# Performance work log

Hardware: AMD Instinct MI355X
Metric: run time of the kernel (lower is better)

## Reference

```python
import jax, jax.numpy as jnp
import numpy as np

B, S, D, H = 4, 2048, 768, 12
HD = D // H
SCALE = HD ** -0.5


def setup_inputs() -> dict:
    key = jax.random.key(0)
    ks = jax.random.split(key, 10)
    inp = {
        "x": jax.random.normal(ks[0], (B, S, D), jnp.float32),
        "attn_mask": jax.random.normal(ks[1], (B, S), jnp.float32),
        "Wq": jax.random.normal(ks[2], (D, D), jnp.float32) * (D ** -0.5),
        "bq": jax.random.normal(ks[3], (D,), jnp.float32) * 0.02,
        "Wk": jax.random.normal(ks[4], (D, D), jnp.float32) * (D ** -0.5),
        "bk": jax.random.normal(ks[5], (D,), jnp.float32) * 0.02,
        "Wv": jax.random.normal(ks[6], (D, D), jnp.float32) * (D ** -0.5),
        "bv": jax.random.normal(ks[7], (D,), jnp.float32) * 0.02,
        "Wo": jax.random.normal(ks[8], (D, D), jnp.float32) * (D ** -0.5),
        "bo": jax.random.normal(ks[9], (D,), jnp.float32) * 0.02,
    }
    return inp


def _split_heads(e):
    # [B, S, D] -> [B, H, S, HD]
    return e.reshape(B, S, H, HD).transpose(0, 2, 1, 3)


def reference(x, attn_mask, Wq, bq, Wk, bk, Wv, bv, Wo, bo):
    q = _split_heads((x @ Wq + bq) * SCALE)          # [B,H,S,HD]
    k = _split_heads(x @ Wk + bk)                     # [B,H,S,HD]
    v = _split_heads(x @ Wv + bv)                     # [B,H,S,HD]
    scores = jnp.einsum('bhsd,bhtd->bhst', q, k)      # [B,H,S,S]
    scores = scores + attn_mask[:, None, None, :]     # additive mask over keys
    probs = jax.nn.softmax(scores, axis=-1)
    out = jnp.einsum('bhst,bhtd->bhsd', probs, v)     # [B,H,S,HD]
    out = out.transpose(0, 2, 1, 3).reshape(B, S, D)  # merge heads
    return out @ Wo + bo
```

## Files before the change

kernel.cpp:

```cpp
#include <hip/hip_runtime.h>
#include <cmath>

#define B_ 4
#define S_ 2048
#define D_ 768
#define H_ 12
#define HD_ 64
#define SCALE_ 0.125f
#define LOG2E_ 1.4426950408889634f
#define M_ 8192

typedef unsigned short ushortT;
typedef unsigned int u32;
typedef __attribute__((ext_vector_type(8))) __bf16 bf16x8;
typedef __attribute__((ext_vector_type(4))) float f32x4;
typedef __attribute__((ext_vector_type(16))) float f32x16;

typedef __attribute__((address_space(1))) const void glb_cv;
typedef __attribute__((address_space(3))) void lds_v;

__device__ inline ushortT f2bf(float f) {
    return __builtin_bit_cast(ushortT, (__bf16)f);
}

__device__ inline u32 pk2bf(float a, float b) {
    return (u32)__builtin_bit_cast(ushortT, (__bf16)a)
         | ((u32)__builtin_bit_cast(ushortT, (__bf16)b) << 16);
}

__device__ inline float sum2bf(u32 u) {
    return __builtin_bit_cast(float, u << 16)
         + __builtin_bit_cast(float, u & 0xffff0000u);
}

__device__ inline void gload_lds16(const void* g, void* l) {
    __builtin_amdgcn_global_load_lds((glb_cv*)g, (lds_v*)l, 16, 0, 0);
}

__global__ __launch_bounds__(256)
void convert_f32_bf16(const float* __restrict__ in, ushortT* __restrict__ out)
{
    const size_t i = ((size_t)blockIdx.x * 256 + threadIdx.x) * 8;
    float4 a = *(const float4*)(in + i);
    float4 b = *(const float4*)(in + i + 4);
    union { ushortT u[8]; float4 f; } o;
    o.u[0] = f2bf(a.x); o.u[1] = f2bf(a.y); o.u[2] = f2bf(a.z); o.u[3] = f2bf(a.w);
    o.u[4] = f2bf(b.x); o.u[5] = f2bf(b.y); o.u[6] = f2bf(b.z); o.u[7] = f2bf(b.w);
    *(float4*)(out + i) = o.f;
}

__global__ __launch_bounds__(256)
void scale_mask(const float* __restrict__ in, float* __restrict__ outp)
{
    const int i = blockIdx.x * 256 + threadIdx.x;
    outp[i] = in[i] * LOG2E_;
}

__global__ __launch_bounds__(256)
void transpose_w(const float* __restrict__ W0, const float* __restrict__ W1,
                 const float* __restrict__ W2, const float* __restrict__ W3,
                 ushortT* __restrict__ wt4)
{
    const float* W = (blockIdx.z == 0) ? W0 : (blockIdx.z == 1) ? W1
                   : (blockIdx.z == 2) ? W2 : W3;
    ushortT* o = wt4 + (size_t)blockIdx.z * 768 * 768;
    __shared__ float T[64][65];
    const int tid = threadIdx.x;
    const int k0 = blockIdx.x * 64, n0 = blockIdx.y * 64;

    for (int t = tid; t < 1024; t += 256) {
        const int r = t >> 4, c4 = (t & 15) << 2;
        float4 v = *(const float4*)&W[(size_t)(k0 + r) * 768 + n0 + c4];
        T[r][c4 + 0] = v.x; T[r][c4 + 1] = v.y;
        T[r][c4 + 2] = v.z; T[r][c4 + 3] = v.w;
    }
    __syncthreads();
    for (int t = tid; t < 1024; t += 256) {
        const int r = t >> 4, c4 = (t & 15) << 2;
        union { ushortT u[4]; unsigned long long v; } ov;
        ov.u[0] = f2bf(T[c4 + 0][r]); ov.u[1] = f2bf(T[c4 + 1][r]);
        ov.u[2] = f2bf(T[c4 + 2][r]); ov.u[3] = f2bf(T[c4 + 3][r]);
        *(unsigned long long*)&o[(size_t)(n0 + r) * 768 + k0 + c4] = ov.v;
    }
}

__device__ inline void gemm_core_128x64(
    const ushortT* __restrict__ A, const ushortT* __restrict__ Bt,
    ushortT* As, ushortT* Bs, int m0, int n0, f32x4 acc[4][2])
{
    const int tid  = threadIdx.x;
    const int lane = tid & 63;
    const int wave = tid >> 6;
    const int lr = lane & 15, lg = lane >> 4;
    const int wr = wave >> 1, wc = wave & 1;

    #pragma unroll
    for (int mi = 0; mi < 4; ++mi)
        #pragma unroll
        for (int ni = 0; ni < 2; ++ni)
            acc[mi][ni] = (f32x4){0.f, 0.f, 0.f, 0.f};

    #pragma unroll 1
    for (int k0 = 0; k0 < 768; k0 += 64) {
        __syncthreads();
        #pragma unroll
        for (int it = 0; it < 4; ++it) {
            const int ci = it * 256 + tid;
            const int row = ci >> 3, c = ci & 7;
            const int sc = c ^ (row & 7);
            gload_lds16(A + (size_t)(m0 + row) * 768 + k0 + sc * 8,
                        As + (size_t)(it * 256 + wave * 64) * 8);
        }
        #pragma unroll
        for (int it = 0; it < 2; ++it) {
            const int ci = it * 256 + tid;
            const int row = ci >> 3, c = ci & 7;
            const int sc = c ^ (row & 7);
            gload_lds16(Bt + (size_t)(n0 + row) * 768 + k0 + sc * 8,
                        Bs + (size_t)(it * 256 + wave * 64) * 8);
        }
        __syncthreads();

        #pragma unroll
        for (int ks = 0; ks < 2; ++ks) {
            bf16x8 af[4], bfr[2];
            #pragma unroll
            for (int mi = 0; mi < 4; ++mi) {
                const int row = wr * 64 + mi * 16 + lr;
                const int ch = (ks * 4 + lg) ^ (row & 7);
                af[mi] = __builtin_bit_cast(bf16x8, *(const float4*)(As + row * 64 + ch * 8));
            }
            #pragma unroll
            for (int ni = 0; ni < 2; ++ni) {
                const int row = wc * 32 + ni * 16 + lr;
                const int ch = (ks * 4 + lg) ^ (row & 7);
                bfr[ni] = __builtin_bit_cast(bf16x8, *(const float4*)(Bs + row * 64 + ch * 8));
            }
            #pragma unroll
            for (int mi = 0; mi < 4; ++mi)
                #pragma unroll
                for (int ni = 0; ni < 2; ++ni)
                    acc[mi][ni] = __builtin_amdgcn_mfma_f32_16x16x32_bf16(
                        af[mi], bfr[ni], acc[mi][ni], 0, 0, 0);
        }
    }
}

__global__ __launch_bounds__(256)
void qkv_gemm(const ushortT* __restrict__ xb, const ushortT* __restrict__ wt4,
              const float* __restrict__ bq, const float* __restrict__ bk,
              const float* __restrict__ bv,
              ushortT* __restrict__ qb, ushortT* __restrict__ kb,
              ushortT* __restrict__ vtb)
{
    __shared__ __align__(16) ushortT As[128 * 64];
    __shared__ __align__(16) ushortT Bs[64 * 64];
    const int z = blockIdx.z;
    const ushortT* Wt = wt4 + (size_t)z * 768 * 768;
    const float* bias = (z == 0) ? bq : (z == 1) ? bk : bv;
    const float scale = (z == 0) ? (SCALE_ * LOG2E_) : 1.0f;

    const int m0 = blockIdx.x * 128, n0 = blockIdx.y * 64;
    f32x4 acc[4][2];
    gemm_core_128x64(xb, Wt, As, Bs, m0, n0, acc);

    const int tid = threadIdx.x;
    const int lane = tid & 63, wave = tid >> 6;
    const int lr = lane & 15, lg = lane >> 4;
    const int wr = wave >> 1, wc = wave & 1;
    const int h = n0 >> 6;

    if (z == 2) {
        #pragma unroll
        for (int ni = 0; ni < 2; ++ni) {
            const int nn = wc * 32 + ni * 16 + lr;
            const float bb = bias[n0 + nn];
            #pragma unroll
            for (int mi = 0; mi < 4; ++mi) {
                const int mb = m0 + wr * 64 + mi * 16 + lg * 4;
                const int b = mb >> 11, s = mb & 2047;
                ushort4 ov;
                ov.x = f2bf(acc[mi][ni][0] + bb);
                ov.y = f2bf(acc[mi][ni][1] + bb);
                ov.z = f2bf(acc[mi][ni][2] + bb);
                ov.w = f2bf(acc[mi][ni][3] + bb);
                *(ushort4*)&vtb[(((size_t)b * H_ + h) * HD_ + nn) * S_ + s] = ov;
            }
        }
    } else {
        ushortT* out = (z == 0) ? qb : kb;
        #pragma unroll
        for (int ni = 0; ni < 2; ++ni) {
            const int nn = wc * 32 + ni * 16 + lr;
            const float bb = bias[n0 + nn];
            #pragma unroll
            for (int mi = 0; mi < 4; ++mi) {
                #pragma unroll
                for (int j = 0; j < 4; ++j) {
                    const int m = m0 + wr * 64 + mi * 16 + lg * 4 + j;
                    const int b = m >> 11, s = m & 2047;
                    out[(((size_t)b * H_ + h) * S_ + s) * HD_ + nn] =
                        f2bf((acc[mi][ni][j] + bb) * scale);
                }
            }
        }
    }
}

__global__ __launch_bounds__(256)
void o_gemm(const ushortT* __restrict__ ab, const ushortT* __restrict__ wto,
            const float* __restrict__ bo, float* __restrict__ out)
{
    __shared__ __align__(16) ushortT As[128 * 64];
    __shared__ __align__(16) ushortT Bs[64 * 64];
    const int m0 = blockIdx.x * 128, n0 = blockIdx.y * 64;
    f32x4 acc[4][2];
    gemm_core_128x64(ab, wto, As, Bs, m0, n0, acc);

    const int tid = threadIdx.x;
    const int lane = tid & 63, wave = tid >> 6;
    const int lr = lane & 15, lg = lane >> 4;
    const int wr = wave >> 1, wc = wave & 1;

    #pragma unroll
    for (int ni = 0; ni < 2; ++ni) {
        const int n = n0 + wc * 32 + ni * 16 + lr;
        const float bb = bo[n];
        #pragma unroll
        for (int mi = 0; mi < 4; ++mi) {
            #pragma unroll
            for (int j = 0; j < 4; ++j) {
                const int m = m0 + wr * 64 + mi * 16 + lg * 4 + j;
                out[(size_t)m * 768 + n] = acc[mi][ni][j] + bb;
            }
        }
    }
}

__global__ __launch_bounds__(128, 2)
void attn_mfma(const ushortT* __restrict__ Q, const ushortT* __restrict__ K,
               const ushortT* __restrict__ Vt, const float* __restrict__ msc,
               ushortT* __restrict__ out)
{
    __shared__ __align__(16) ushortT Ks[2][64 * 64];
    __shared__ __align__(16) ushortT Vs[2][64 * 64];

    const int tid  = threadIdx.x;
    const int lane = tid & 63;
    const int wq   = tid >> 6;
    const int col  = lane & 31;
    const int hi   = lane >> 5;

    const int gid  = blockIdx.x;
    const int xcd  = gid & 7;
    const int w    = gid >> 3;
    const int bh_i = xcd * 6 + (w >> 4);
    const int q0   = (w & 15) * 128;
    const int b    = bh_i / H_;
    const int h    = bh_i % H_;
    const size_t bh = (size_t)bh_i;

    bf16x8 qf[2][4];
    #pragma unroll
    for (int qb2 = 0; qb2 < 2; ++qb2) {
        const ushortT* Qg = Q + (bh * S_ + q0 + wq * 64 + qb2 * 32 + col) * HD_;
        #pragma unroll
        for (int ks = 0; ks < 4; ++ks)
            qf[qb2][ks] = __builtin_bit_cast(bf16x8,
                *(const float4*)(Qg + ks * 16 + hi * 8));
    }

    const ushortT* Kg = K  + bh * S_ * HD_;
    const ushortT* Vg = Vt + bh * HD_ * S_;
    const float*   mg = msc + (size_t)b * S_;

    const ushortT* ksrc[4];
    const ushortT* vsrc[4];
    #pragma unroll
    for (int it = 0; it < 4; ++it) {
        const int ci = it * 128 + tid;
        const int row = ci >> 3, c = ci & 7, sc = c ^ (row & 7);
        ksrc[it] = Kg + (size_t)row * HD_ + sc * 8;
        vsrc[it] = Vg + (size_t)row * S_ + sc * 8;
    }

    int ko[2][4], vo[2][4];
    #pragma unroll
    for (int kb2 = 0; kb2 < 2; ++kb2) {
        const int r = kb2 * 32 + col;
        #pragma unroll
        for (int ks = 0; ks < 4; ++ks)
            ko[kb2][ks] = r * 128 + (((2 * ks + hi) ^ (r & 7)) << 4);
    }
    #pragma unroll
    for (int hb = 0; hb < 2; ++hb) {
        const int r = hb * 32 + col;
        #pragma unroll
        for (int sg = 0; sg < 4; ++sg)
            vo[hb][sg] = r * 128 + (((2 * sg + hi) ^ (r & 7)) << 4);
    }

    f32x16 acc[2][2];
    float accl[2] = {0.f, 0.f};
    #pragma unroll
    for (int qb2 = 0; qb2 < 2; ++qb2)
        #pragma unroll
        for (int hb = 0; hb < 2; ++hb)
            #pragma unroll
            for (int r = 0; r < 16; ++r) acc[qb2][hb][r] = 0.f;

    auto stage = [&](int bsel) {
        #pragma unroll
        for (int it = 0; it < 4; ++it) {
            gload_lds16(ksrc[it], &Ks[bsel][(it * 128 + wq * 64) * 8]);
            ksrc[it] += 64 * HD_;
        }
        #pragma unroll
        for (int it = 0; it < 4; ++it) {
            gload_lds16(vsrc[it], &Vs[bsel][(it * 128 + wq * 64) * 8]);
            vsrc[it] += 64;
        }
    };

    stage(0);
    __syncthreads();

    for (int kt = 0; kt < S_ / 64; ++kt) {
        const int buf = kt & 1;
        if (kt + 1 < S_ / 64) stage(buf ^ 1);

        f32x16 cin[2];
        #pragma unroll
        for (int kb2 = 0; kb2 < 2; ++kb2) {
            #pragma unroll
            for (int g = 0; g < 4; ++g) {
                float4 mv = *(const float4*)(mg + kt * 64 + kb2 * 32 + g * 8 + hi * 4);
                cin[kb2][4 * g + 0] = mv.x;
                cin[kb2][4 * g + 1] = mv.y;
                cin[kb2][4 * g + 2] = mv.z;
                cin[kb2][4 * g + 3] = mv.w;
            }
        }

        bf16x8 kf[2][4];
        #pragma unroll
        for (int kb2 = 0; kb2 < 2; ++kb2)
            #pragma unroll
            for (int ks = 0; ks < 4; ++ks)
                kf[kb2][ks] = __builtin_bit_cast(bf16x8,
                    *(const float4*)((const char*)&Ks[buf][0] + ko[kb2][ks]));

        bf16x8 vf[2][4];
        #pragma unroll
        for (int hb = 0; hb < 2; ++hb)
            #pragma unroll
            for (int sg = 0; sg < 4; ++sg)
                vf[hb][sg] = __builtin_bit_cast(bf16x8,
                    *(const float4*)((const char*)&Vs[buf][0] + vo[hb][sg]));

        #pragma unroll
        for (int qb2 = 0; qb2 < 2; ++qb2) {
            u32 bw[4][4];
            float lsum = 0.f;
            #pragma unroll
            for (int kb2 = 0; kb2 < 2; ++kb2) {
                f32x16 s = cin[kb2];
                __builtin_amdgcn_s_setprio(1);
                #pragma unroll
                for (int ks = 0; ks < 4; ++ks)
                    s = __builtin_amdgcn_mfma_f32_32x32x16_bf16(
                        kf[kb2][ks], qf[qb2][ks], s, 0, 0, 0);
                __builtin_amdgcn_s_setprio(0);

                float p[16];
                #pragma unroll
                for (int r = 0; r < 16; ++r) p[r] = exp2f(s[r]);

                #pragma unroll
                for (int sl = 0; sl < 2; ++sl) {
                    u32 u0 = pk2bf(p[8 * sl + 0], p[8 * sl + 1]);
                    u32 u1 = pk2bf(p[8 * sl + 2], p[8 * sl + 3]);
                    u32 v0 = pk2bf(p[8 * sl + 4], p[8 * sl + 5]);
                    u32 v1 = pk2bf(p[8 * sl + 6], p[8 * sl + 7]);
                    lsum += (sum2bf(u0) + sum2bf(u1)) + (sum2bf(v0) + sum2bf(v1));
                    asm("v_permlane32_swap_b32 %0, %1" : "+v"(u0), "+v"(v0));
                    asm("v_permlane32_swap_b32 %0, %1" : "+v"(u1), "+v"(v1));
                    const int sg = kb2 * 2 + sl;
                    bw[sg][0] = u0; bw[sg][1] = u1;
                    bw[sg][2] = v0; bw[sg][3] = v1;
                }
            }
            accl[qb2] += lsum + __shfl_xor(lsum, 32);

            __builtin_amdgcn_s_setprio(1);
            #pragma unroll
            for (int sg = 0; sg < 4; ++sg) {
                union { u32 w[4]; bf16x8 v; } pb;
                pb.w[0] = bw[sg][0]; pb.w[1] = bw[sg][1];
                pb.w[2] = bw[sg][2]; pb.w[3] = bw[sg][3];
                #pragma unroll
                for (int hb = 0; hb < 2; ++hb)
                    acc[qb2][hb] = __builtin_amdgcn_mfma_f32_32x32x16_bf16(
                        vf[hb][sg], pb.v, acc[qb2][hb], 0, 0, 0);
            }
            __builtin_amdgcn_s_setprio(0);
        }

        __syncthreads();
    }

    #pragma unroll
    for (int qb2 = 0; qb2 < 2; ++qb2) {
        const float inv = 1.f / accl[qb2];
        const size_t row = (size_t)b * S_ + q0 + wq * 64 + qb2 * 32 + col;
        #pragma unroll
        for (int hb = 0; hb < 2; ++hb) {
            #pragma unroll
            for (int t = 0; t < 4; ++t) {
                ushort4 ov;
                ov.x = f2bf(acc[qb2][hb][4 * t + 0] * inv);
                ov.y = f2bf(acc[qb2][hb][4 * t + 1] * inv);
                ov.z = f2bf(acc[qb2][hb][4 * t + 2] * inv);
                ov.w = f2bf(acc[qb2][hb][4 * t + 3] * inv);
                *(ushort4*)&out[row * D_ + h * HD_ + hb * 32 + t * 8 + hi * 4] = ov;
            }
        }
    }
}

extern "C" void kernel_launch(void* const* d_in, const int* in_sizes, int n_in,
                              void* d_out, int out_size, void* d_ws, size_t ws_size,
                              hipStream_t stream)
{
    const float* x    = (const float*)d_in[0];
    const float* mask = (const float*)d_in[1];
    const float* Wq   = (const float*)d_in[2];
    const float* bq   = (const float*)d_in[3];
    const float* Wk   = (const float*)d_in[4];
    const float* bk   = (const float*)d_in[5];
    const float* Wv   = (const float*)d_in[6];
    const float* bv   = (const float*)d_in[7];
    const float* Wo   = (const float*)d_in[8];
    const float* bo   = (const float*)d_in[9];
    float* out = (float*)d_out;

    const size_t NE = (size_t)B_ * S_ * D_;
    ushortT* xb  = (ushortT*)d_ws;
    ushortT* qb  = xb + NE;
    ushortT* kb  = qb + NE;
    ushortT* vtb = kb + NE;
    ushortT* ab  = vtb + NE;
    ushortT* wt4 = ab + NE;
    float*   msc = (float*)(wt4 + (size_t)4 * 768 * 768);

    convert_f32_bf16<<<NE / 2048, 256, 0, stream>>>(x, xb);
    scale_mask<<<(B_ * S_) / 256, 256, 0, stream>>>(mask, msc);
    transpose_w<<<dim3(12, 12, 4), 256, 0, stream>>>(Wq, Wk, Wv, Wo, wt4);

    qkv_gemm<<<dim3(M_ / 128, 12, 3), 256, 0, stream>>>(
        xb, wt4, bq, bk, bv, qb, kb, vtb);

    attn_mfma<<<768, 128, 0, stream>>>(qb, kb, vtb, msc, ab);

    o_gemm<<<dim3(M_ / 128, 12), 256, 0, stream>>>(
        ab, wt4 + (size_t)3 * 768 * 768, bo, out);
}
```

Baseline: 210.0 us.

## Split attention key range in two and add a partial-combine kernel

Each attention block now covers only half of the key sequence, which doubles the grid to 1536 blocks. Each block writes unnormalized bf16 partial outputs plus per-row softmax denominators. A new combine kernel sums the two partials and divides by the summed denominators before the output projection, and the launch bound is raised to four blocks per CU. The aim is better CU load balance and occupancy. The cost is an extra pass over two activation-sized buffers, extra bf16 rounding of the partials, and possible register pressure or spills from the tighter launch bound.

```diff
diff --git a/kernel.cpp b/kernel.cpp
--- a/kernel.cpp
+++ b/kernel.cpp
@@ -9,6 +9,7 @@
 #define SCALE_ 0.125f
 #define LOG2E_ 1.4426950408889634f
 #define M_ 8192
+#define NE_ 6291456ull
 
 typedef unsigned short ushortT;
 typedef unsigned int u32;
@@ -21,6 +22,10 @@
 
 __device__ inline ushortT f2bf(float f) {
     return __builtin_bit_cast(ushortT, (__bf16)f);
+}
+
+__device__ inline float bf2f(ushortT u) {
+    return __builtin_bit_cast(float, (u32)u << 16);
 }
 
 __device__ inline u32 pk2bf(float a, float b) {
@@ -237,10 +242,10 @@
     }
 }
 
-__global__ __launch_bounds__(128, 2)
+__global__ __launch_bounds__(128, 4)
 void attn_mfma(const ushortT* __restrict__ Q, const ushortT* __restrict__ K,
                const ushortT* __restrict__ Vt, const float* __restrict__ msc,
-               ushortT* __restrict__ out)
+               ushortT* __restrict__ pn, float* __restrict__ pl)
 {
     __shared__ __align__(16) ushortT Ks[2][64 * 64];
     __shared__ __align__(16) ushortT Vs[2][64 * 64];
@@ -254,8 +259,10 @@
     const int gid  = blockIdx.x;
     const int xcd  = gid & 7;
     const int w    = gid >> 3;
-    const int bh_i = xcd * 6 + (w >> 4);
-    const int q0   = (w & 15) * 128;
+    const int bh_i = xcd * 6 + (w >> 5);
+    const int r5   = w & 31;
+    const int q0   = (r5 >> 1) * 128;
+    const int kh   = r5 & 1;
     const int b    = bh_i / H_;
     const int h    = bh_i % H_;
     const size_t bh = (size_t)bh_i;
@@ -270,9 +277,9 @@
                 *(const float4*)(Qg + ks * 16 + hi * 8));
     }
 
-    const ushortT* Kg = K  + bh * S_ * HD_;
-    const ushortT* Vg = Vt + bh * HD_ * S_;
-    const float*   mg = msc + (size_t)b * S_;
+    const ushortT* Kg = K  + bh * S_ * HD_ + (size_t)kh * 1024 * HD_;
+    const ushortT* Vg = Vt + bh * HD_ * S_ + (size_t)kh * 1024;
+    const float*   mg = msc + (size_t)b * S_ + (size_t)kh * 1024;
 
     const ushortT* ksrc[4];
     const ushortT* vsrc[4];
@@ -325,9 +332,9 @@
     stage(0);
     __syncthreads();
 
-    for (int kt = 0; kt < S_ / 64; ++kt) {
+    for (int kt = 0; kt < 16; ++kt) {
         const int buf = kt & 1;
-        if (kt + 1 < S_ / 64) stage(buf ^ 1);
+        if (kt + 1 < 16) stage(buf ^ 1);
 
         f32x16 cin[2];
         #pragma unroll
@@ -409,23 +416,48 @@
         __syncthreads();
     }
 
+    ushortT* pnh = pn + (size_t)kh * NE_;
+    float*   plh = pl + (size_t)kh * B_ * H_ * S_;
     #pragma unroll
     for (int qb2 = 0; qb2 < 2; ++qb2) {
-        const float inv = 1.f / accl[qb2];
-        const size_t row = (size_t)b * S_ + q0 + wq * 64 + qb2 * 32 + col;
+        const int q = q0 + wq * 64 + qb2 * 32 + col;
+        const size_t row = (size_t)b * S_ + q;
+        plh[bh * S_ + q] = accl[qb2];
         #pragma unroll
         for (int hb = 0; hb < 2; ++hb) {
             #pragma unroll
             for (int t = 0; t < 4; ++t) {
                 ushort4 ov;
-                ov.x = f2bf(acc[qb2][hb][4 * t + 0] * inv);
-                ov.y = f2bf(acc[qb2][hb][4 * t + 1] * inv);
-                ov.z = f2bf(acc[qb2][hb][4 * t + 2] * inv);
-                ov.w = f2bf(acc[qb2][hb][4 * t + 3] * inv);
-                *(ushort4*)&out[row * D_ + h * HD_ + hb * 32 + t * 8 + hi * 4] = ov;
-            }
-        }
-    }
+                ov.x = f2bf(acc[qb2][hb][4 * t + 0]);
+                ov.y = f2bf(acc[qb2][hb][4 * t + 1]);
+                ov.z = f2bf(acc[qb2][hb][4 * t + 2]);
+                ov.w = f2bf(acc[qb2][hb][4 * t + 3]);
+                *(ushort4*)&pnh[row * D_ + h * HD_ + hb * 32 + t * 8 + hi * 4] = ov;
+            }
+        }
+    }
+}
+
+__global__ __launch_bounds__(256)
+void combine(const ushortT* __restrict__ pn, const float* __restrict__ pl,
+             ushortT* __restrict__ ab)
+{
+    const size_t i8 = ((size_t)blockIdx.x * 256 + threadIdx.x) * 8;
+    const int d   = (int)(i8 % D_);
+    const size_t row = i8 / D_;
+    const int hh  = d >> 6;
+    const int b   = (int)(row >> 11);
+    const int s   = (int)(row & 2047);
+    const size_t li = ((size_t)b * H_ + hh) * S_ + s;
+    const float inv = 1.f / (pl[li] + pl[(size_t)B_ * H_ * S_ + li]);
+
+    union { ushortT u[8]; float4 f; } a, c, o;
+    a.f = *(const float4*)(pn + i8);
+    c.f = *(const float4*)(pn + NE_ + i8);
+    #pragma unroll
+    for (int j = 0; j < 8; ++j)
+        o.u[j] = f2bf((bf2f(a.u[j]) + bf2f(c.u[j])) * inv);
+    *(float4*)(ab + i8) = o.f;
 }
 
 extern "C" void kernel_launch(void* const* d_in, const int* in_sizes, int n_in,
@@ -444,23 +476,26 @@
     const float* bo   = (const float*)d_in[9];
     float* out = (float*)d_out;
 
-    const size_t NE = (size_t)B_ * S_ * D_;
     ushortT* xb  = (ushortT*)d_ws;
-    ushortT* qb  = xb + NE;
-    ushortT* kb  = qb + NE;
-    ushortT* vtb = kb + NE;
-    ushortT* ab  = vtb + NE;
-    ushortT* wt4 = ab + NE;
+    ushortT* qb  = xb + NE_;
+    ushortT* kb  = qb + NE_;
+    ushortT* vtb = kb + NE_;
+    ushortT* pn  = vtb + NE_;
+    ushortT* wt4 = pn + 2 * NE_;
     float*   msc = (float*)(wt4 + (size_t)4 * 768 * 768);
-
-    convert_f32_bf16<<<NE / 2048, 256, 0, stream>>>(x, xb);
+    float*   pl  = msc + (size_t)B_ * S_;
+    ushortT* ab  = xb;
+
+    convert_f32_bf16<<<NE_ / 2048, 256, 0, stream>>>(x, xb);
     scale_mask<<<(B_ * S_) / 256, 256, 0, stream>>>(mask, msc);
     transpose_w<<<dim3(12, 12, 4), 256, 0, stream>>>(Wq, Wk, Wv, Wo, wt4);
 
     qkv_gemm<<<dim3(M_ / 128, 12, 3), 256, 0, stream>>>(
         xb, wt4, bq, bk, bv, qb, kb, vtb);
 
-    attn_mfma<<<768, 128, 0, stream>>>(qb, kb, vtb, msc, ab);
+    attn_mfma<<<1536, 128, 0, stream>>>(qb, kb, vtb, msc, pn, pl);
+
+    combine<<<NE_ / 2048, 256, 0, stream>>>(pn, pl, ab);
 
     o_gemm<<<dim3(M_ / 128, 12), 256, 0, stream>>>(
         ab, wt4 + (size_t)3 * 768 * 768, bo, out);
```

New measurement: 217.4 us. +3.5%, slower.

## Split attention block into four 32-row waves and compute row sums via MFMA

Applied to the files above, without the earlier changes.

The attention kernel now runs 256 threads per block, with each wave owning 32 query rows instead of 64. This halves the per-wave Q fragments and accumulators, and K/V fragments are loaded from LDS right before use instead of being held in registers for the whole tile. The softmax denominator is now computed by an extra MFMA against a ones vector rather than scalar bf16 unpacking, adds and a cross-lane shuffle. The aim is lower register pressure, higher occupancy and less VALU work, at the cost of each K/V LDS tile feeding fewer query rows per wave and more barrier participants.

```diff
diff --git a/kernel.cpp b/kernel.cpp
--- a/kernel.cpp
+++ b/kernel.cpp
@@ -9,6 +9,7 @@
 #define SCALE_ 0.125f
 #define LOG2E_ 1.4426950408889634f
 #define M_ 8192
+#define NE_ 6291456ull
 
 typedef unsigned short ushortT;
 typedef unsigned int u32;
@@ -26,11 +27,6 @@
 __device__ inline u32 pk2bf(float a, float b) {
     return (u32)__builtin_bit_cast(ushortT, (__bf16)a)
          | ((u32)__builtin_bit_cast(ushortT, (__bf16)b) << 16);
-}
-
-__device__ inline float sum2bf(u32 u) {
-    return __builtin_bit_cast(float, u << 16)
-         + __builtin_bit_cast(float, u & 0xffff0000u);
 }
 
 __device__ inline void gload_lds16(const void* g, void* l) {
@@ -237,7 +233,7 @@
     }
 }
 
-__global__ __launch_bounds__(128, 2)
+__global__ __launch_bounds__(256, 3)
 void attn_mfma(const ushortT* __restrict__ Q, const ushortT* __restrict__ K,
                const ushortT* __restrict__ Vt, const float* __restrict__ msc,
                ushortT* __restrict__ out)
@@ -260,13 +256,12 @@
     const int h    = bh_i % H_;
     const size_t bh = (size_t)bh_i;
 
-    bf16x8 qf[2][4];
-    #pragma unroll
-    for (int qb2 = 0; qb2 < 2; ++qb2) {
-        const ushortT* Qg = Q + (bh * S_ + q0 + wq * 64 + qb2 * 32 + col) * HD_;
+    bf16x8 qf[4];
+    {
+        const ushortT* Qg = Q + (bh * S_ + q0 + wq * 32 + col) * HD_;
         #pragma unroll
         for (int ks = 0; ks < 4; ++ks)
-            qf[qb2][ks] = __builtin_bit_cast(bf16x8,
+            qf[ks] = __builtin_bit_cast(bf16x8,
                 *(const float4*)(Qg + ks * 16 + hi * 8));
     }
 
@@ -274,11 +269,11 @@
     const ushortT* Vg = Vt + bh * HD_ * S_;
     const float*   mg = msc + (size_t)b * S_;
 
-    const ushortT* ksrc[4];
-    const ushortT* vsrc[4];
-    #pragma unroll
-    for (int it = 0; it < 4; ++it) {
-        const int ci = it * 128 + tid;
+    const ushortT* ksrc[2];
+    const ushortT* vsrc[2];
+    #pragma unroll
+    for (int it = 0; it < 2; ++it) {
+        const int ci = it * 256 + tid;
         const int row = ci >> 3, c = ci & 7, sc = c ^ (row & 7);
         ksrc[it] = Kg + (size_t)row * HD_ + sc * 8;
         vsrc[it] = Vg + (size_t)row * S_ + sc * 8;
@@ -300,24 +295,28 @@
             vo[hb][sg] = r * 128 + (((2 * sg + hi) ^ (r & 7)) << 4);
     }
 
-    f32x16 acc[2][2];
-    float accl[2] = {0.f, 0.f};
-    #pragma unroll
-    for (int qb2 = 0; qb2 < 2; ++qb2)
-        #pragma unroll
-        for (int hb = 0; hb < 2; ++hb)
-            #pragma unroll
-            for (int r = 0; r < 16; ++r) acc[qb2][hb][r] = 0.f;
+    bf16x8 onesA;
+    #pragma unroll
+    for (int i = 0; i < 8; ++i) onesA[i] = (__bf16)1.0f;
+
+    f32x16 acc[2];
+    f32x16 accl;
+    #pragma unroll
+    for (int hb = 0; hb < 2; ++hb)
+        #pragma unroll
+        for (int r = 0; r < 16; ++r) acc[hb][r] = 0.f;
+    #pragma unroll
+    for (int r = 0; r < 16; ++r) accl[r] = 0.f;
 
     auto stage = [&](int bsel) {
         #pragma unroll
-        for (int it = 0; it < 4; ++it) {
-            gload_lds16(ksrc[it], &Ks[bsel][(it * 128 + wq * 64) * 8]);
+        for (int it = 0; it < 2; ++it) {
+            gload_lds16(ksrc[it], &Ks[bsel][(it * 256 + wq * 64) * 8]);
             ksrc[it] += 64 * HD_;
         }
         #pragma unroll
-        for (int it = 0; it < 4; ++it) {
-            gload_lds16(vsrc[it], &Vs[bsel][(it * 128 + wq * 64) * 8]);
+        for (int it = 0; it < 2; ++it) {
+            gload_lds16(vsrc[it], &Vs[bsel][(it * 256 + wq * 64) * 8]);
             vsrc[it] += 64;
         }
     };
@@ -329,101 +328,80 @@
         const int buf = kt & 1;
         if (kt + 1 < S_ / 64) stage(buf ^ 1);
 
-        f32x16 cin[2];
+        u32 bw[4][4];
         #pragma unroll
         for (int kb2 = 0; kb2 < 2; ++kb2) {
+            f32x16 s;
             #pragma unroll
             for (int g = 0; g < 4; ++g) {
                 float4 mv = *(const float4*)(mg + kt * 64 + kb2 * 32 + g * 8 + hi * 4);
-                cin[kb2][4 * g + 0] = mv.x;
-                cin[kb2][4 * g + 1] = mv.y;
-                cin[kb2][4 * g + 2] = mv.z;
-                cin[kb2][4 * g + 3] = mv.w;
-            }
-        }
-
-        bf16x8 kf[2][4];
-        #pragma unroll
-        for (int kb2 = 0; kb2 < 2; ++kb2)
-            #pragma unroll
-            for (int ks = 0; ks < 4; ++ks)
-                kf[kb2][ks] = __builtin_bit_cast(bf16x8,
+                s[4 * g + 0] = mv.x;
+                s[4 * g + 1] = mv.y;
+                s[4 * g + 2] = mv.z;
+                s[4 * g + 3] = mv.w;
+            }
+
+            __builtin_amdgcn_s_setprio(1);
+            #pragma unroll
+            for (int ks = 0; ks < 4; ++ks) {
+                bf16x8 kf = __builtin_bit_cast(bf16x8,
                     *(const float4*)((const char*)&Ks[buf][0] + ko[kb2][ks]));
-
-        bf16x8 vf[2][4];
-        #pragma unroll
-        for (int hb = 0; hb < 2; ++hb)
-            #pragma unroll
-            for (int sg = 0; sg < 4; ++sg)
-                vf[hb][sg] = __builtin_bit_cast(bf16x8,
+                s = __builtin_amdgcn_mfma_f32_32x32x16_bf16(
+                    kf, qf[ks], s, 0, 0, 0);
+            }
+            __builtin_amdgcn_s_setprio(0);
+
+            float p[16];
+            #pragma unroll
+            for (int r = 0; r < 16; ++r) p[r] = exp2f(s[r]);
+
+            #pragma unroll
+            for (int sl = 0; sl < 2; ++sl) {
+                u32 u0 = pk2bf(p[8 * sl + 0], p[8 * sl + 1]);
+                u32 u1 = pk2bf(p[8 * sl + 2], p[8 * sl + 3]);
+                u32 v0 = pk2bf(p[8 * sl + 4], p[8 * sl + 5]);
+                u32 v1 = pk2bf(p[8 * sl + 6], p[8 * sl + 7]);
+                asm("v_permlane32_swap_b32 %0, %1" : "+v"(u0), "+v"(v0));
+                asm("v_permlane32_swap_b32 %0, %1" : "+v"(u1), "+v"(v1));
+                const int sg = kb2 * 2 + sl;
+                bw[sg][0] = u0; bw[sg][1] = u1;
+                bw[sg][2] = v0; bw[sg][3] = v1;
+            }
+        }
+
+        __builtin_amdgcn_s_setprio(1);
+        #pragma unroll
+        for (int sg = 0; sg < 4; ++sg) {
+            union { u32 w[4]; bf16x8 v; } pb;
+            pb.w[0] = bw[sg][0]; pb.w[1] = bw[sg][1];
+            pb.w[2] = bw[sg][2]; pb.w[3] = bw[sg][3];
+            #pragma unroll
+            for (int hb = 0; hb < 2; ++hb) {
+                bf16x8 vf = __builtin_bit_cast(bf16x8,
                     *(const float4*)((const char*)&Vs[buf][0] + vo[hb][sg]));
-
-        #pragma unroll
-        for (int qb2 = 0; qb2 < 2; ++qb2) {
-            u32 bw[4][4];
-            float lsum = 0.f;
-            #pragma unroll
-            for (int kb2 = 0; kb2 < 2; ++kb2) {
-                f32x16 s = cin[kb2];
-                __builtin_amdgcn_s_setprio(1);
-                #pragma unroll
-                for (int ks = 0; ks < 4; ++ks)
-                    s = __builtin_amdgcn_mfma_f32_32x32x16_bf16(
-                        kf[kb2][ks], qf[qb2][ks], s, 0, 0, 0);
-                __builtin_amdgcn_s_setprio(0);
-
-                float p[16];
-                #pragma unroll
-                for (int r = 0; r < 16; ++r) p[r] = exp2f(s[r]);
-
-                #pragma unroll
-                for (int sl = 0; sl < 2; ++sl) {
-                    u32 u0 = pk2bf(p[8 * sl + 0], p[8 * sl + 1]);
-                    u32 u1 = pk2bf(p[8 * sl + 2], p[8 * sl + 3]);
-                    u32 v0 = pk2bf(p[8 * sl + 4], p[8 * sl + 5]);
-                    u32 v1 = pk2bf(p[8 * sl + 6], p[8 * sl + 7]);
-                    lsum += (sum2bf(u0) + sum2bf(u1)) + (sum2bf(v0) + sum2bf(v1));
-                    asm("v_permlane32_swap_b32 %0, %1" : "+v"(u0), "+v"(v0));
-                    asm("v_permlane32_swap_b32 %0, %1" : "+v"(u1), "+v"(v1));
-                    const int sg = kb2 * 2 + sl;
-                    bw[sg][0] = u0; bw[sg][1] = u1;
-                    bw[sg][2] = v0; bw[sg][3] = v1;
-                }
-            }
-            accl[qb2] += lsum + __shfl_xor(lsum, 32);
-
-            __builtin_amdgcn_s_setprio(1);
-            #pragma unroll
-            for (int sg = 0; sg < 4; ++sg) {
-                union { u32 w[4]; bf16x8 v; } pb;
-                pb.w[0] = bw[sg][0]; pb.w[1] = bw[sg][1];
-                pb.w[2] = bw[sg][2]; pb.w[3] = bw[sg][3];
-                #pragma unroll
-                for (int hb = 0; hb < 2; ++hb)
-                    acc[qb2][hb] = __builtin_amdgcn_mfma_f32_32x32x16_bf16(
-                        vf[hb][sg], pb.v, acc[qb2][hb], 0, 0, 0);
-            }
-            __builtin_amdgcn_s_setprio(0);
-        }
+                acc[hb] = __builtin_amdgcn_mfma_f32_32x32x16_bf16(
+                    vf, pb.v, acc[hb], 0, 0, 0);
+            }
+            accl = __builtin_amdgcn_mfma_f32_32x32x16_bf16(
+                onesA, pb.v, accl, 0, 0, 0);
+        }
+        __builtin_amdgcn_s_setprio(0);
 
         __syncthreads();
     }
 
-    #pragma unroll
-    for (int qb2 = 0; qb2 < 2; ++qb2) {
-        const float inv = 1.f / accl[qb2];
-        const size_t row = (size_t)b * S_ + q0 + wq * 64 + qb2 * 32 + col;
-        #pragma unroll
-        for (int hb = 0; hb < 2; ++hb) {
-            #pragma unroll
-            for (int t = 0; t < 4; ++t) {
-                ushort4 ov;
-                ov.x = f2bf(acc[qb2][hb][4 * t + 0] * inv);
-                ov.y = f2bf(acc[qb2][hb][4 * t + 1] * inv);
-                ov.z = f2bf(acc[qb2][hb][4 * t + 2] * inv);
-                ov.w = f2bf(acc[qb2][hb][4 * t + 3] * inv);
-                *(ushort4*)&out[row * D_ + h * HD_ + hb * 32 + t * 8 + hi * 4] = ov;
-            }
+    const float inv = 1.f / accl[0];
+    const size_t row = (size_t)b * S_ + q0 + wq * 32 + col;
+    #pragma unroll
+    for (int hb = 0; hb < 2; ++hb) {
+        #pragma unroll
+        for (int t = 0; t < 4; ++t) {
+            ushort4 ov;
+            ov.x = f2bf(acc[hb][4 * t + 0] * inv);
+            ov.y = f2bf(acc[hb][4 * t + 1] * inv);
+            ov.z = f2bf(acc[hb][4 * t + 2] * inv);
+            ov.w = f2bf(acc[hb][4 * t + 3] * inv);
+            *(ushort4*)&out[row * D_ + h * HD_ + hb * 32 + t * 8 + hi * 4] = ov;
         }
     }
 }
@@ -444,23 +422,22 @@
     const float* bo   = (const float*)d_in[9];
     float* out = (float*)d_out;
 
-    const size_t NE = (size_t)B_ * S_ * D_;
     ushortT* xb  = (ushortT*)d_ws;
-    ushortT* qb  = xb + NE;
-    ushortT* kb  = qb + NE;
-    ushortT* vtb = kb + NE;
-    ushortT* ab  = vtb + NE;
-    ushortT* wt4 = ab + NE;
+    ushortT* qb  = xb + NE_;
+    ushortT* kb  = qb + NE_;
+    ushortT* vtb = kb + NE_;
+    ushortT* ab  = vtb + NE_;
+    ushortT* wt4 = ab + NE_;
     float*   msc = (float*)(wt4 + (size_t)4 * 768 * 768);
 
-    convert_f32_bf16<<<NE / 2048, 256, 0, stream>>>(x, xb);
+    convert_f32_bf16<<<NE_ / 2048, 256, 0, stream>>>(x, xb);
     scale_mask<<<(B_ * S_) / 256, 256, 0, stream>>>(mask, msc);
     transpose_w<<<dim3(12, 12, 4), 256, 0, stream>>>(Wq, Wk, Wv, Wo, wt4);
 
     qkv_gemm<<<dim3(M_ / 128, 12, 3), 256, 0, stream>>>(
         xb, wt4, bq, bk, bv, qb, kb, vtb);
 
-    attn_mfma<<<768, 128, 0, stream>>>(qb, kb, vtb, msc, ab);
+    attn_mfma<<<768, 256, 0, stream>>>(qb, kb, vtb, msc, ab);
 
     o_gemm<<<dim3(M_ / 128, 12), 256, 0, stream>>>(
         ab, wt4 + (size_t)3 * 768 * 768, bo, out);
```

New measurement: 171.2 us, median of 2. 18.5% less time.
